# Performance work log

Measured on AMD Instinct MI355X. Metric: run time of the kernel, lower is better.

## Reference

```python
import jax, jax.numpy as jnp
from jax import lax
import numpy as np

B, S, E, HID = 16, 7, 64, 64
RES = (64, 64); D = RES[0] * RES[1]
XLOW, XHIGH = -0.5, 0.5
RLOW, RHIGH = float(np.sqrt(0.01)), float(np.sqrt(0.05))
PIXEL_MULT = 1.0; N_ITER = 3; TSOFT = 1.0 / float(np.sqrt(E))

def _build_grid():
    ranges = [np.linspace(XLOW, XHIGH, r) for r in RES]
    g = np.stack(np.meshgrid(*ranges, indexing='xy'), axis=-1)
    g = g.reshape(RES[0], RES[1], -1).reshape(1, -1, 2)
    return jnp.asarray(g, dtype=jnp.float32)

ABS_GRID = _build_grid()  # [1, D, 2]

def _ln(x, g, b):
    m = jnp.mean(x, -1, keepdims=True)
    v = jnp.mean(jnp.square(x - m), -1, keepdims=True)
    return (x - m) * lax.rsqrt(v + 1e-5) * g + b

def _forward(data, slot_noise, pos_rand, conv0_w, conv0_b, conv1_w, conv1_b, conv2_w, conv2_b,
             dataN_g, dataN_b, queryN_g, queryN_b, toK_w, toK_b, toV_w, toV_b, dense_w, dense_b,
             mlp1_w, mlp1_b, mlp2_w, mlp2_b, gru_wih, gru_whh, gru_bih, gru_bhh,
             alpha1_w, alpha1_b, alpha2_w, alpha2_b, final1_w, final1_b, final2_w, final2_b,
             slots_mu, slots_logsigma):
    dn = ('NCHW', 'OIHW', 'NCHW')
    def conv(x, w, b):
        return lax.conv_general_dilated(x, w, (1, 1), 'SAME', dimension_numbers=dn) + b[None, :, None, None]
    # CNN encoder: Conv-ReLU x3, 'same' padding, k=5
    x = jax.nn.relu(conv(data, conv0_w, conv0_b))
    x = jax.nn.relu(conv(x, conv1_w, conv1_b))
    x = jax.nn.relu(conv(x, conv2_w, conv2_b))
    enc = x.transpose(0, 2, 3, 1).reshape(B, D, HID)
    enc = _ln(enc, dataN_g, dataN_b)

    queries = slots_mu + jnp.exp(slots_logsigma) * slot_noise  # [B,S,E]
    # init_slots: faithful replication (source indexes the SLOT dim, and swaps rlow/rhigh)
    pos_scale = pos_rand.at[:, :2, :].add(-0.5)
    pos_scale = pos_scale.at[:, -1, :].set((RLOW - RHIGH) * pos_rand[:, -1, :] + RHIGH)

    encK = enc @ toK_w + toK_b  # [B,D,E]
    encV = enc @ toV_w + toV_b

    def init_mlp(y):
        y = _ln(y, queryN_g, queryN_b)
        return jax.nn.relu(y @ mlp1_w + mlp1_b) @ mlp2_w + mlp2_b

    def get_kv(ps):
        # per-slot relative grid: [B,S,D,2]
        rel = (ABS_GRID[:, None] - ps[:, :, None, :2]) / ps[:, :, -1][:, :, None, None]
        eg = PIXEL_MULT * (rel @ dense_w + dense_b)  # [B,S,D,E]
        return init_mlp(encK[:, None] + eg), init_mlp(encV[:, None] + eg)

    def att_wts(q, k):
        logits = jnp.einsum('bse,bsde->bsd', q, k) * TSOFT
        att = jax.nn.softmax(logits, axis=1)  # softmax over slots
        wts = att / jnp.sum(att, -1, keepdims=True) + 1e-8
        return att, wts

    def update_frames(wts):
        new_pos = jnp.einsum('bsd,de->bse', wts, ABS_GRID[0])  # [B,S,2]
        d2 = jnp.sum(jnp.square(ABS_GRID[:, None] - new_pos[:, :, None]), -1)  # [B,S,D]
        new_scale = jnp.sqrt(jnp.einsum('bsd,bsd->bs', wts, d2))
        return jnp.concatenate([new_pos, new_scale[..., None]], -1)

    def gru(xg, h):
        gi = xg @ gru_wih.T + gru_bih
        gh = h @ gru_whh.T + gru_bhh
        ir, iz, inn = jnp.split(gi, 3, -1)
        hr, hz, hn = jnp.split(gh, 3, -1)
        r = jax.nn.sigmoid(ir + hr)
        z = jax.nn.sigmoid(iz + hz)
        n = jnp.tanh(inn + r * hn)
        return (1.0 - z) * n + z * h

    for _ in range(N_ITER):
        keys, vals = get_kv(pos_scale)
        att, wts = att_wts(_ln(queries, queryN_g, queryN_b), keys)
        pos_scale = update_frames(wts)
        upd = jnp.einsum('bsd,bsde->bse', wts, vals)
        queries = gru(upd.reshape(-1, E), queries.reshape(-1, E)).reshape(B, S, E)

    keys, _ = get_kv(pos_scale)
    att, wts = att_wts(_ln(queries, queryN_g, queryN_b), keys)
    nps = update_frames(wts)
    alpha = jax.nn.sigmoid(jax.nn.relu(queries @ alpha1_w + alpha1_b) @ alpha2_w + alpha2_b)
    slot_feat = jax.nn.relu(queries @ final1_w + final1_b) @ final2_w + final2_b + nps
    return queries, att, slot_feat, alpha

def setup_inputs() -> dict:
    ks = jax.random.split(jax.random.key(0), 20)
    f32 = jnp.float32
    def rn(i, shape, s):
        return jax.random.normal(ks[i], shape, f32) * s
    inp = dict(
        data=jax.random.normal(ks[0], (B, 1, RES[0], RES[1]), f32),
        slot_noise=jax.random.normal(ks[1], (B, S, E), f32),
        pos_rand=jax.random.uniform(ks[2], (B, S, 3), dtype=f32),
        conv0_w=rn(3, (HID, 1, 5, 5), 0.2), conv0_b=jnp.zeros(HID, f32),
        conv1_w=rn(4, (HID, HID, 5, 5), 0.025), conv1_b=jnp.zeros(HID, f32),
        conv2_w=rn(5, (HID, HID, 5, 5), 0.025), conv2_b=jnp.zeros(HID, f32),
        dataN_g=jnp.ones(HID, f32), dataN_b=jnp.zeros(HID, f32),
        queryN_g=jnp.ones(E, f32), queryN_b=jnp.zeros(E, f32),
        toK_w=rn(6, (HID, E), 0.125), toK_b=jnp.zeros(E, f32),
        toV_w=rn(7, (HID, E), 0.125), toV_b=jnp.zeros(E, f32),
        dense_w=rn(8, (2, E), 0.7), dense_b=jnp.zeros(E, f32),
        mlp1_w=rn(9, (E, E), 0.125), mlp1_b=jnp.zeros(E, f32),
        mlp2_w=rn(10, (E, E), 0.125), mlp2_b=jnp.zeros(E, f32),
        gru_wih=rn(11, (3 * E, E), 0.125), gru_whh=rn(12, (3 * E, E), 0.125),
        gru_bih=jnp.zeros(3 * E, f32), gru_bhh=jnp.zeros(3 * E, f32),
        alpha1_w=rn(13, (E, 32), 0.125), alpha1_b=jnp.zeros(32, f32),
        alpha2_w=rn(14, (32, 1), 0.18), alpha2_b=jnp.zeros(1, f32),
        final1_w=rn(15, (E, HID), 0.125), final1_b=jnp.zeros(HID, f32),
        final2_w=rn(16, (HID, 3), 0.125), final2_b=jnp.zeros(3, f32),
        slots_mu=rn(17, (1, 1, E), 1.0),
        slots_logsigma=rn(18, (1, 1, E), 0.01),
    )
    return inp

def reference(data, slot_noise, pos_rand, conv0_w, conv0_b, conv1_w, conv1_b, conv2_w, conv2_b,
              dataN_g, dataN_b, queryN_g, queryN_b, toK_w, toK_b, toV_w, toV_b, dense_w, dense_b,
              mlp1_w, mlp1_b, mlp2_w, mlp2_b, gru_wih, gru_whh, gru_bih, gru_bhh,
              alpha1_w, alpha1_b, alpha2_w, alpha2_b, final1_w, final1_b, final2_w, final2_b,
              slots_mu, slots_logsigma):
    return _forward(data, slot_noise, pos_rand, conv0_w, conv0_b, conv1_w, conv1_b, conv2_w, conv2_b,
                    dataN_g, dataN_b, queryN_g, queryN_b, toK_w, toK_b, toV_w, toV_b, dense_w, dense_b,
                    mlp1_w, mlp1_b, mlp2_w, mlp2_b, gru_wih, gru_whh, gru_bih, gru_bhh,
                    alpha1_w, alpha1_b, alpha2_w, alpha2_b, final1_w, final1_b, final2_w, final2_b,
                    slots_mu, slots_logsigma)
```

## Files before the change

kernel.cpp:

```cpp
#include <hip/hip_runtime.h>
#include <cmath>


#define RLOW_F 0.1f
#define RHIGH_F 0.22360679774997896f
#define W0CONST 1.00004096f
#define SR2 704.3386243f

typedef __attribute__((ext_vector_type(8))) __bf16 bf16x8;
typedef __attribute__((ext_vector_type(4))) float f32x4;

__device__ __forceinline__ float wsum64(float v){
  #pragma unroll
  for (int off = 32; off > 0; off >>= 1) v += __shfl_xor(v, off, 64);
  return v;
}
__device__ __forceinline__ float rdlane(float v, int l){
  return __int_as_float(__builtin_amdgcn_readlane(__float_as_int(v), l));
}
__device__ __forceinline__ unsigned short bf16bits(float v){
  __bf16 h = (__bf16)v;
  return *reinterpret_cast<unsigned short*>(&h);
}

// ... 61 lines not shown
    int yy = y + r - 2, gx = cx - 2;
    float v = 0.f;
    if (yy >= 0 && yy < 64 && gx >= 0 && gx < 64) v = in[(b*64 + yy)*64 + gx];
    s_in[r*68 + cx] = v;
  }
  __syncthreads();
  int o = lane;
  float bvv = bias[o];
  float acc[16];
  #pragma unroll
  for (int k = 0; k < 16; k++) acc[k] = bvv;
  #pragma unroll
  for (int ky = 0; ky < 5; ky++){
    float rv[20];
    const float4* p = reinterpret_cast<const float4*>(&s_in[ky*68 + xg*16]);
    #pragma unroll
    for (int q = 0; q < 5; q++){ float4 f = p[q]; rv[q*4]=f.x; rv[q*4+1]=f.y; rv[q*4+2]=f.z; rv[q*4+3]=f.w; }
    #pragma unroll
    for (int kx = 0; kx < 5; kx++){
      float wv = s_w[o*25 + ky*5 + kx];
      #pragma unroll
      for (int k = 0; k < 16; k++) acc[k] = fmaf(rv[k+kx], wv, acc[k]);
    }
  }
  #pragma unroll
  for (int k = 0; k < 16; k++) s_out[o*65 + xg*16 + k] = fmaxf(acc[k], 0.f);
  __syncthreads();
  for (int i = t; i < 4096; i += 256){
    int px = i >> 6, ch = i & 63;
    out[((size_t)(b*64 + y)*64 + px)*64 + ch] = bf16bits(s_out[ch*65 + px]);
  }
}

__global__ void k_packconv(const float* __restrict__ w, unsigned short* __restrict__ out){
  int idx = blockIdx.x*256 + threadIdx.x;
  if (idx >= 102400) return;
  int j = idx & 7;
  int l = (idx >> 3) & 63;
  int frag = idx >> 9;
  int nt = frag & 3;
  int ks = (frag >> 2) % 10;
  int dy = frag / 40;
  int q = l >> 4, cr = l & 15;
  int k = ks*32 + q*8 + j;
  int kx = k >> 6, ch = k & 63;
  int n = nt*16 + cr;
  out[idx] = bf16bits(w[((n*64 + ch)*5 + dy)*5 + kx]);
}

__global__ __launch_bounds__(256) void k_convm(const unsigned short* __restrict__ in_bf,
                        const unsigned short* __restrict__ wpack,
                        const float* __restrict__ bias,
                        const float* __restrict__ lng, const float* __restrict__ lnb,
                        unsigned short* __restrict__ out_bf, float* __restrict__ out_f,
                        int mode){
  int bi = blockIdx.x;
  int b = bi >> 4; int yg = bi & 15;
  int t = threadIdx.x; int wv = t >> 6; int l = t & 63;
  int q = l >> 4, cr = l & 15;
  int p0 = wv*16;

  __shared__ char lds[8*68*144];

  for (int ri = 0; ri < 8; ri++){
    int yy = yg*4 + ri - 2;
    bool rok = (yy >= 0 && yy < 64);
    const uint4* src = reinterpret_cast<const uint4*>(in_bf + (size_t)(b*64 + yy)*64*64);
    for (int i = t; i < 544; i += 256){
      int px = i >> 3, c8 = i & 7;
      uint4 v = {0u,0u,0u,0u};
      int gx = px - 2;
      if (rok && gx >= 0 && gx < 64) v = src[gx*8 + c8];
      *reinterpret_cast<uint4*>(&lds[ri*9792 + px*144 + c8*16]) = v;
    }
  }
  __syncthreads();

  f32x4 acc[4][4];
  #pragma unroll
  for (int r = 0; r < 4; r++)
    #pragma unroll
    for (int nt = 0; nt < 4; nt++) acc[r][nt] = (f32x4){0.f,0.f,0.f,0.f};

  const bf16x8* wp = reinterpret_cast<const bf16x8*>(wpack);
  for (int dy = 0; dy < 5; dy++){
    for (int ks = 0; ks < 10; ks++){
      bf16x8 Bf[4];
      int fbase = (dy*10 + ks)*4;
      #pragma unroll
      for (int nt = 0; nt < 4; nt++) Bf[nt] = wp[(fbase + nt)*64 + l];
      int aoff = (p0 + cr + (ks >> 1))*144 + (ks & 1)*64 + q*16;
      #pragma unroll
      for (int r = 0; r < 4; r++){
        bf16x8 a = *reinterpret_cast<const bf16x8*>(&lds[(r + dy)*9792 + aoff]);
        #pragma unroll
        for (int nt = 0; nt < 4; nt++)
          acc[r][nt] = __builtin_amdgcn_mfma_f32_16x16x32_bf16(a, Bf[nt], acc[r][nt], 0, 0, 0);
      }
    }
  }

  float bvv[4];
  #pragma unroll
  for (int nt = 0; nt < 4; nt++) bvv[nt] = bias[nt*16 + cr];

  if (mode == 0){
    #pragma unroll
    for (int r = 0; r < 4; r++){
      int y = yg*4 + r;
      #pragma unroll
      for (int reg = 0; reg < 4; reg++){
        int p = p0 + q*4 + reg;
        size_t base = ((size_t)(b*64 + y)*64 + p)*64;
        #pragma unroll
        for (int nt = 0; nt < 4; nt++)
          out_bf[base + nt*16 + cr] = bf16bits(fmaxf(acc[r][nt][reg] + bvv[nt], 0.f));
      }
    }
  } else {
    float gv[4], bb[4];
    #pragma unroll
    for (int nt = 0; nt < 4; nt++){ gv[nt] = lng[nt*16 + cr]; bb[nt] = lnb[nt*16 + cr]; }
    #pragma unroll
    for (int r = 0; r < 4; r++){
      int y = yg*4 + r;
      #pragma unroll
      for (int reg = 0; reg < 4; reg++){
        int p = p0 + q*4 + reg;
        float v[4]; float s1 = 0.f, s2 = 0.f;
        #pragma unroll
        for (int nt = 0; nt < 4; nt++){
          v[nt] = fmaxf(acc[r][nt][reg] + bvv[nt], 0.f);
          s1 += v[nt]; s2 += v[nt]*v[nt];
        }
        #pragma unroll
        for (int m = 1; m < 16; m <<= 1){ s1 += __shfl_xor(s1, m, 64); s2 += __shfl_xor(s2, m, 64); }
        float mean = s1 * (1.f/64.f);
        float var  = s2 * (1.f/64.f) - mean*mean;
        float rstd = 1.0f/sqrtf(var + 1e-5f);
        size_t base = ((size_t)b*4096 + y*64 + p)*64;
        #pragma unroll
        for (int nt = 0; nt < 4; nt++)
          out_f[base + nt*16 + cr] = (v[nt] - mean)*rstd*gv[nt] + bb[nt];
      }
    }
  }
}

__global__ void k_packw1(const float* __restrict__ w1, unsigned short* __restrict__ out){
  int idx = blockIdx.x*256 + threadIdx.x;
  int jj = idx & 7;
  int lane = (idx >> 3) & 63;
  int frag = idx >> 9;
  int ks = frag >> 2, nt = frag & 3;
  int q = lane >> 4, cr = lane & 15;
  int k = ks*32 + q*8 + jj;
  int n = nt*16 + cr;
  out[idx] = bf16bits(w1[k*64 + n]);
}

__global__ __launch_bounds__(256) void k_projm(const float* __restrict__ enc,
                       const unsigned short* __restrict__ kpack, const float* __restrict__ bk,
                       const unsigned short* __restrict__ vpack, const float* __restrict__ bvp,
                       unsigned short* __restrict__ K, unsigned short* __restrict__ V){
  int bi = blockIdx.x; int b = bi >> 6; int tile = bi & 63;
  int t = threadIdx.x; int wv = t >> 6; int l = t & 63;
  int q = l >> 4, cr = l & 15;
  int d0 = tile*64 + wv*16;

  const bf16x8* kp = reinterpret_cast<const bf16x8*>(kpack);
  const bf16x8* vp = reinterpret_cast<const bf16x8*>(vpack);
  bf16x8 KB[8], VB[8];
  #pragma unroll
  for (int f = 0; f < 8; f++){ KB[f] = kp[f*64 + l]; VB[f] = vp[f*64 + l]; }

  const float* er = enc + (size_t)(b*4096 + d0 + cr)*64;
  bf16x8 a0, a1;
  #pragma unroll
  for (int h = 0; h < 2; h++){
    const float4* e4 = reinterpret_cast<const float4*>(er + (h ? (32 + q*8) : (q*8)));
    #pragma unroll
    for (int p = 0; p < 2; p++){
      float4 e = e4[p];
      if (h == 0){ a0[p*4+0]=(__bf16)e.x; a0[p*4+1]=(__bf16)e.y; a0[p*4+2]=(__bf16)e.z; a0[p*4+3]=(__bf16)e.w; }
      else       { a1[p*4+0]=(__bf16)e.x; a1[p*4+1]=(__bf16)e.y; a1[p*4+2]=(__bf16)e.z; a1[p*4+3]=(__bf16)e.w; }
    }
  }

  f32x4 zero = {0.f,0.f,0.f,0.f};
  f32x4 aK[4], aV[4];
  #pragma unroll
  for (int nt = 0; nt < 4; nt++){
    aK[nt] = __builtin_amdgcn_mfma_f32_16x16x32_bf16(a0, KB[nt],     zero,   0, 0, 0);
    aK[nt] = __builtin_amdgcn_mfma_f32_16x16x32_bf16(a1, KB[4 + nt], aK[nt], 0, 0, 0);
    aV[nt] = __builtin_amdgcn_mfma_f32_16x16x32_bf16(a0, VB[nt],     zero,   0, 0, 0);
    aV[nt] = __builtin_amdgcn_mfma_f32_16x16x32_bf16(a1, VB[4 + nt], aV[nt], 0, 0, 0);
  }
  #pragma unroll
  for (int nt = 0; nt < 4; nt++){
    float bkv = bk[nt*16 + cr], bvv = bvp[nt*16 + cr];
    #pragma unroll
    for (int reg = 0; reg < 4; reg++){
      size_t base = ((size_t)b*4096 + d0 + q*4 + reg)*64 + nt*16 + cr;
      K[base] = bf16bits(aK[nt][reg] + bkv);
      V[base] = bf16bits(aV[nt][reg] + bvv);
    }
  }
}

__global__ __launch_bounds__(256) void k_attnK(const unsigned short* __restrict__ encX,
     const unsigned short* __restrict__ w1pack, const float* __restrict__ mlp1b,
     const float* __restrict__ absc, const float* __restrict__ qg_,
     const float* __restrict__ qb_, const float* __restrict__ w2qc,
     float* __restrict__ att, float* __restrict__ accF){
  int bi = blockIdx.x;
  int b = bi >> 6, tile = bi & 63;
  int t = threadIdx.x; int wv = t >> 6; int l = t & 63;
  int q = l >> 4, cr = l & 15;
  int m0 = tile*64 + wv*16;
  int drow = m0 + cr;

  __shared__ float s_log[7*64];
  __shared__ float s_absc[7*192];
  __shared__ float s_wq[7*68];
  for (int i = t; i < 1344; i += 256) s_absc[i] = absc[b*7*192 + i];
  for (int i = t; i < 476;  i += 256) s_wq[i]   = w2qc[b*7*68 + i];

  const bf16x8* wp = reinterpret_cast<const bf16x8*>(w1pack);
  bf16x8 Bf[8];
  #pragma unroll
  for (int f = 0; f < 8; f++) Bf[f] = wp[f*64 + l];

  const unsigned short* er = encX + (size_t)(b*4096 + drow)*64;
  float gx = -0.5f + (float)(drow & 63) * (1.f/63.f);
  float gy = -0.5f + (float)((drow >> 6) & 63) * (1.f/63.f);
  float xb[16], gq[16], bq[16];
  {
    bf16x8 ea = *reinterpret_cast<const bf16x8*>(er + q*8);
    bf16x8 eb = *reinterpret_cast<const bf16x8*>(er + 32 + q*8);
    #pragma unroll
    for (int i = 0; i < 8; i++){ xb[i] = (float)ea[i]; xb[8+i] = (float)eb[i]; }
  }
  #pragma unroll
  for (int h = 0; h < 2; h++){
    int fb = h ? (32 + q*8) : (q*8);
    const float4* g4 = reinterpret_cast<const float4*>(qg_ + fb);
    const float4* b4 = reinterpret_cast<const float4*>(qb_ + fb);
    #pragma unroll
    for (int p = 0; p < 2; p++){
      float4 gg = g4[p], bb = b4[p];
      int o = h*8 + p*4;
      gq[o+0]=gg.x; gq[o+1]=gg.y; gq[o+2]=gg.z; gq[o+3]=gg.w;
      bq[o+0]=bb.x; bq[o+1]=bb.y; bq[o+2]=bb.z; bq[o+3]=bb.w;
    }
  }
  float b1v[4];
  #pragma unroll
  for (int nt = 0; nt < 4; nt++) b1v[nt] = mlp1b[nt*16 + cr];
  __syncthreads();

  for (int s = 0; s < 7; s++){
    const float* Ac = s_absc + s*192;
    float x[16];
    #pragma unroll
    for (int h = 0; h < 2; h++){
      int fb = h ? (32 + q*8) : (q*8);
      const float4* A4 = reinterpret_cast<const float4*>(Ac + fb);
      const float4* B4 = reinterpret_cast<const float4*>(Ac + 64 + fb);
      const float4* C4 = reinterpret_cast<const float4*>(Ac + 128 + fb);
      #pragma unroll
      for (int p = 0; p < 2; p++){
        float4 Av = A4[p], Bv = B4[p], Cv = C4[p];
        int o = h*8 + p*4;
        x[o+0] = xb[o+0] + gx*Av.x + gy*Bv.x + Cv.x;
        x[o+1] = xb[o+1] + gx*Av.y + gy*Bv.y + Cv.y;
        x[o+2] = xb[o+2] + gx*Av.z + gy*Bv.z + Cv.z;
        x[o+3] = xb[o+3] + gx*Av.w + gy*Bv.w + Cv.w;
      }
    }
    float sum = 0.f;
    #pragma unroll
    for (int k = 0; k < 16; k++) sum += x[k];
    sum += __shfl_xor(sum, 16, 64); sum += __shfl_xor(sum, 32, 64);
    float m = sum * (1.f/64.f);
    float v = 0.f;
    #pragma unroll
    for (int k = 0; k < 16; k++){ float dd = x[k] - m; v += dd*dd; }
    v += __shfl_xor(v, 16, 64); v += __shfl_xor(v, 32, 64);
    float rstd = 1.0f/sqrtf(v * (1.f/64.f) + 1e-5f);

    bf16x8 a0, a1;
    #pragma unroll
    for (int k = 0; k < 8; k++)  a0[k] = (__bf16)((x[k]   - m)*rstd*gq[k]   + bq[k]);
    #pragma unroll
    for (int k = 0; k < 8; k++)  a1[k] = (__bf16)((x[8+k] - m)*rstd*gq[8+k] + bq[8+k]);

    f32x4 zero = {0.f, 0.f, 0.f, 0.f};
    f32x4 acc[4];
    #pragma unroll
    for (int nt = 0; nt < 4; nt++){
      acc[nt] = __builtin_amdgcn_mfma_f32_16x16x32_bf16(a0, Bf[nt],     zero,    0, 0, 0);
      acc[nt] = __builtin_amdgcn_mfma_f32_16x16x32_bf16(a1, Bf[4 + nt], acc[nt], 0, 0, 0);
    }

    float c2 = s_wq[s*68 + 64];
    float p[4] = {0.f, 0.f, 0.f, 0.f};
    #pragma unroll
    for (int nt = 0; nt < 4; nt++){
      float wqv = s_wq[s*68 + nt*16 + cr];
      #pragma unroll
      for (int reg = 0; reg < 4; reg++){
        float y = fmaxf(acc[nt][reg] + b1v[nt], 0.f);
        p[reg] = fmaf(y, wqv, p[reg]);
      }
    }
    #pragma unroll
    for (int reg = 0; reg < 4; reg++){
      #pragma unroll
      for (int off = 1; off < 16; off <<= 1) p[reg] += __shfl_xor(p[reg], off, 64);
    }
    if (cr == 0){
      #pragma unroll
      for (int reg = 0; reg < 4; reg++)
        s_log[s*64 + wv*16 + q*4 + reg] = (p[reg] + c2) * 0.125f;
    }
  }
  __syncthreads();

  if (t < 64){
    float lv[7];
    #pragma unroll
    for (int s = 0; s < 7; s++) lv[s] = s_log[s*64 + t];
    float mx = lv[0];
    #pragma unroll
    for (int s = 1; s < 7; s++) mx = fmaxf(mx, lv[s]);
    float sm = 0.f;
    #pragma unroll
    for (int s = 0; s < 7; s++){ lv[s] = expf(lv[s] - mx); sm += lv[s]; }
    float inv = 1.0f / sm;
    #pragma unroll
    for (int s = 0; s < 7; s++){
      float a = lv[s] * inv;
      s_log[s*64 + t] = a;
      att[(size_t)(b*7+s)*4096 + tile*64 + t] = a;
    }
  }
  __syncthreads();

  if (t < 224){
    int s = t >> 5, r = t & 31;
    float a1 = s_log[s*64 + r];
    float a2 = s_log[s*64 + r + 32];
    float gx1 = -0.5f + (float)r * (1.f/63.f);
    float gx2 = -0.5f + (float)(r + 32) * (1.f/63.f);
    float gyc = -0.5f + (float)tile * (1.f/63.f);
    float gy2c = gyc*gyc;
    float w0 = a1 + a2;
    float w1 = a1*gx1 + a2*gx2;
    float w2 = w0*gyc;
    float w3 = a1*(gx1*gx1 + gy2c) + a2*(gx2*gx2 + gy2c);
    #pragma unroll
    for (int m = 1; m < 32; m <<= 1){
      w0 += __shfl_xor(w0, m, 64);
      w1 += __shfl_xor(w1, m, 64);
      w2 += __shfl_xor(w2, m, 64);
      w3 += __shfl_xor(w3, m, 64);
    }
    if (r == 0){
      atomicAdd(&accF[(b*7+s)*4 + 0], w0);
      atomicAdd(&accF[(b*7+s)*4 + 1], w1);
      atomicAdd(&accF[(b*7+s)*4 + 2], w2);
      atomicAdd(&accF[(b*7+s)*4 + 3], w3);
    }
  }
}

__global__ __launch_bounds__(256) void k_attnV(const unsigned short* __restrict__ encX,
     const unsigned short* __restrict__ w1pack, const float* __restrict__ mlp1b,
     const float* __restrict__ absc, const float* __restrict__ qg_,
     const float* __restrict__ qb_, const float* __restrict__ att,
     const float* __restrict__ accF, float* __restrict__ upd){
  int bi = blockIdx.x;
  int b = bi >> 6, tile = bi & 63;
  int t = threadIdx.x; int wv = t >> 6; int l = t & 63;
  int q = l >> 4, cr = l & 15;
  int m0 = tile*64 + wv*16;
  int drow = m0 + cr;

  __shared__ float s_absc[7*192];
  __shared__ float s_att[7*64];
  __shared__ float s_upd[7*64];
  __shared__ float s_inv[7];
  for (int i = t; i < 1344; i += 256) s_absc[i] = absc[b*7*192 + i];
  for (int i = t; i < 448;  i += 256){
    s_att[i] = att[(size_t)(b*7 + (i >> 6))*4096 + tile*64 + (i & 63)];
    s_upd[i] = 0.f;
  }
  if (t < 7) s_inv[t] = 1.0f / accF[(b*7 + t)*4];

  const bf16x8* wp = reinterpret_cast<const bf16x8*>(w1pack);
  bf16x8 Bf[8];
  #pragma unroll
  for (int f = 0; f < 8; f++) Bf[f] = wp[f*64 + l];

  const unsigned short* er = encX + (size_t)(b*4096 + drow)*64;
  float gx = -0.5f + (float)(drow & 63) * (1.f/63.f);
  float gy = -0.5f + (float)((drow >> 6) & 63) * (1.f/63.f);
  float xb[16], gq[16], bq[16];
  {
    bf16x8 ea = *reinterpret_cast<const bf16x8*>(er + q*8);
    bf16x8 eb = *reinterpret_cast<const bf16x8*>(er + 32 + q*8);
    #pragma unroll
    for (int i = 0; i < 8; i++){ xb[i] = (float)ea[i]; xb[8+i] = (float)eb[i]; }
  }
  #pragma unroll
  for (int h = 0; h < 2; h++){
    int fb = h ? (32 + q*8) : (q*8);
    const float4* g4 = reinterpret_cast<const float4*>(qg_ + fb);
    const float4* b4 = reinterpret_cast<const float4*>(qb_ + fb);
    #pragma unroll
    for (int p = 0; p < 2; p++){
      float4 gg = g4[p], bb = b4[p];
      int o = h*8 + p*4;
      gq[o+0]=gg.x; gq[o+1]=gg.y; gq[o+2]=gg.z; gq[o+3]=gg.w;
      bq[o+0]=bb.x; bq[o+1]=bb.y; bq[o+2]=bb.z; bq[o+3]=bb.w;
    }
  }
  float b1v[4];
  #pragma unroll
  for (int nt = 0; nt < 4; nt++) b1v[nt] = mlp1b[nt*16 + cr];
  __syncthreads();

  for (int s = 0; s < 7; s++){
    const float* Ac = s_absc + s*192;
    float x[16];
    #pragma unroll
    for (int h = 0; h < 2; h++){
      int fb = h ? (32 + q*8) : (q*8);
      const float4* A4 = reinterpret_cast<const float4*>(Ac + fb);
      const float4* B4 = reinterpret_cast<const float4*>(Ac + 64 + fb);
      const float4* C4 = reinterpret_cast<const float4*>(Ac + 128 + fb);
      #pragma unroll
      for (int p = 0; p < 2; p++){
        float4 Av = A4[p], Bv = B4[p], Cv = C4[p];
        int o = h*8 + p*4;
        x[o+0] = xb[o+0] + gx*Av.x + gy*Bv.x + Cv.x;
        x[o+1] = xb[o+1] + gx*Av.y + gy*Bv.y + Cv.y;
        x[o+2] = xb[o+2] + gx*Av.z + gy*Bv.z + Cv.z;
        x[o+3] = xb[o+3] + gx*Av.w + gy*Bv.w + Cv.w;
      }
    }
    float sum = 0.f;
    #pragma unroll
    for (int k = 0; k < 16; k++) sum += x[k];
    sum += __shfl_xor(sum, 16, 64); sum += __shfl_xor(sum, 32, 64);
    float m = sum * (1.f/64.f);
    float v = 0.f;
    #pragma unroll
    for (int k = 0; k < 16; k++){ float dd = x[k] - m; v += dd*dd; }
    v += __shfl_xor(v, 16, 64); v += __shfl_xor(v, 32, 64);
    float rstd = 1.0f/sqrtf(v * (1.f/64.f) + 1e-5f);

    bf16x8 a0, a1;
    #pragma unroll
    for (int k = 0; k < 8; k++)  a0[k] = (__bf16)((x[k]   - m)*rstd*gq[k]   + bq[k]);
    #pragma unroll
    for (int k = 0; k < 8; k++)  a1[k] = (__bf16)((x[8+k] - m)*rstd*gq[8+k] + bq[8+k]);

    f32x4 zero = {0.f, 0.f, 0.f, 0.f};
    f32x4 acc[4];
    #pragma unroll
    for (int nt = 0; nt < 4; nt++){
      acc[nt] = __builtin_amdgcn_mfma_f32_16x16x32_bf16(a0, Bf[nt],     zero,    0, 0, 0);
      acc[nt] = __builtin_amdgcn_mfma_f32_16x16x32_bf16(a1, Bf[4 + nt], acc[nt], 0, 0, 0);
    }

    float rsa = s_inv[s];
    float wr[4];
    #pragma unroll
    for (int reg = 0; reg < 4; reg++)
      wr[reg] = fmaf(s_att[s*64 + wv*16 + q*4 + reg], rsa, 1e-8f);
    float pc[4];
    #pragma unroll
    for (int nt = 0; nt < 4; nt++){
      pc[nt] = 0.f;
      #pragma unroll
      for (int reg = 0; reg < 4; reg++)
        pc[nt] = fmaf(wr[reg], fmaxf(acc[nt][reg] + b1v[nt], 0.f), pc[nt]);
    }
    #pragma unroll
    for (int nt = 0; nt < 4; nt++){
      pc[nt] += __shfl_xor(pc[nt], 16, 64);
      pc[nt] += __shfl_xor(pc[nt], 32, 64);
    }
    if (q == 0){
      #pragma unroll
      for (int nt = 0; nt < 4; nt++)
        atomicAdd(&s_upd[s*64 + nt*16 + cr], pc[nt]);
    }
  }
  __syncthreads();
  for (int i = t; i < 448; i += 256)
    atomicAdd(&upd[b*448 + i], s_upd[i]);
}

__global__ void k_gru(float* __restrict__ upd, float* __restrict__ queries,
                      const float* __restrict__ wih, const float* __restrict__ whh,
                      const float* __restrict__ bih, const float* __restrict__ bhh,
                      const float* __restrict__ mlp2w, const float* __restrict__ mlp2b,
                      float* __restrict__ accF, float* __restrict__ ps,
                      const float* __restrict__ qg_, const float* __restrict__ qb_,
                      const float* __restrict__ dw, const float* __restrict__ db,
                      float* __restrict__ absc, float* __restrict__ w2qc){
  int row = blockIdx.x; int t = threadIdx.x;
  __shared__ float us[64], hs[64], xs[64], gis[192], ghs[192];
  __shared__ float s_ps3[3];
  if (t < 64){ us[t] = upd[row*64 + t]; hs[t] = queries[row*64 + t]; }
  if (t == 64){
    float sa = accF[row*4+0];
    float ax = accF[row*4+1], ay = accF[row*4+2], ar2 = accF[row*4+3];
    float isa = 1.0f/sa;
    float Wx = ax*isa, Wy = ay*isa;
    float Wg = ar2*isa + 1e-8f*SR2;
    float s2 = Wg - (Wx*Wx + Wy*Wy)*(2.f - W0CONST);
    s_ps3[0] = Wx; s_ps3[1] = Wy; s_ps3[2] = sqrtf(fmaxf(s2, 0.f));
  }
  __syncthreads();
  if (t < 64){
    float a = W0CONST * mlp2b[t];
    for (int i = 0; i < 64; i++) a = fmaf(us[i], mlp2w[i*64 + t], a);
    xs[t] = a;
  }
  __syncthreads();
  float gi = bih[t], gh = bhh[t];
  for (int e = 0; e < 64; e++){
    gi = fmaf(wih[t*64 + e], xs[e], gi);
    gh = fmaf(whh[t*64 + e], hs[e], gh);
  }
  gis[t] = gi; ghs[t] = gh;
  __syncthreads();
  if (t < 64){
    float r = 1.0f/(1.0f + expf(-(gis[t]      + ghs[t])));
    float z = 1.0f/(1.0f + expf(-(gis[64+t]   + ghs[64+t])));
    float n = tanhf(gis[128+t] + r*ghs[128+t]);
    float newq = (1.0f - z)*n + z*hs[t];
    queries[row*64 + t] = newq;
    upd[row*64 + t] = 0.f;
    if (t < 4) accF[row*4 + t] = 0.f;
    if (t < 3) ps[row*3 + t] = s_ps3[t];
    pp_core(row, t, newq, s_ps3[0], s_ps3[1], s_ps3[2],
            qg_, qb_, dw, db, mlp2w, mlp2b, absc, w2qc);
  }
}

__global__ void k_final(const float* __restrict__ queries, const float* __restrict__ accF,
                        const float* __restrict__ a1w, const float* __restrict__ a1b,
// ... 44 lines not shown
  const float* conv0_b     = (const float*)d_in[4];
  const float* conv1_w     = (const float*)d_in[5];
  const float* conv1_b     = (const float*)d_in[6];
  const float* conv2_w     = (const float*)d_in[7];
  const float* conv2_b     = (const float*)d_in[8];
  const float* dataN_g     = (const float*)d_in[9];
  const float* dataN_b     = (const float*)d_in[10];
  const float* queryN_g    = (const float*)d_in[11];
  const float* queryN_b    = (const float*)d_in[12];
  const float* toK_w       = (const float*)d_in[13];
  const float* toK_b       = (const float*)d_in[14];
  const float* toV_w       = (const float*)d_in[15];
  const float* toV_b       = (const float*)d_in[16];
  const float* dense_w     = (const float*)d_in[17];
  const float* dense_b     = (const float*)d_in[18];
  const float* mlp1_w      = (const float*)d_in[19];
  const float* mlp1_b      = (const float*)d_in[20];
  const float* mlp2_w      = (const float*)d_in[21];
  const float* mlp2_b      = (const float*)d_in[22];
  const float* gru_wih     = (const float*)d_in[23];
  const float* gru_whh     = (const float*)d_in[24];
  const float* gru_bih     = (const float*)d_in[25];
  const float* gru_bhh     = (const float*)d_in[26];
  const float* alpha1_w    = (const float*)d_in[27];
  const float* alpha1_b    = (const float*)d_in[28];
  const float* alpha2_w    = (const float*)d_in[29];
  const float* alpha2_b    = (const float*)d_in[30];
  const float* final1_w    = (const float*)d_in[31];
  const float* final1_b    = (const float*)d_in[32];
  const float* final2_w    = (const float*)d_in[33];
  const float* final2_b    = (const float*)d_in[34];
  const float* slots_mu    = (const float*)d_in[35];
  const float* slots_lsig  = (const float*)d_in[36];

  float* ws   = (float*)d_ws;
  float* bufA = ws;
  float* bufB = bufA + 4194304;
  float* bufC = bufB + 4194304;
  float* attw = bufC + 4194304;
  float* queries = attw + 458752;
  float* ps   = queries + 7168;
  float* absc = ps + 512;
  float* accF = absc + 21504;
  float* upd  = accF + 512;
  float* w2qc = upd + 7168;
  unsigned short* w1pack = (unsigned short*)(w2qc + 7616);
  unsigned short* kpack  = w1pack + 4096;
  unsigned short* vpack  = kpack + 4096;
  unsigned short* wp1    = vpack + 4096;
  unsigned short* wp2    = wp1 + 102400;

  unsigned short* c0_bf = (unsigned short*)bufA;
  unsigned short* c1_bf = (unsigned short*)bufC;
  float* enc = bufB;
  unsigned short* encK = (unsigned short*)bufA;
  unsigned short* encV = (unsigned short*)bufC;

  float* outq   = (float*)d_out;
  float* outatt = outq + 7168;

  k_prep<<<112, 64, 0, stream>>>(slot_noise, pos_rand, slots_mu, slots_lsig,
                                 queryN_g, queryN_b, dense_w, dense_b, mlp2_w, mlp2_b,
                                 queries, ps, absc, w2qc, accF, upd);
  k_packw1<<<16, 256, 0, stream>>>(mlp1_w, w1pack);
  k_packw1<<<16, 256, 0, stream>>>(toK_w, kpack);
  k_packw1<<<16, 256, 0, stream>>>(toV_w, vpack);
  k_packconv<<<400, 256, 0, stream>>>(conv1_w, wp1);
  k_packconv<<<400, 256, 0, stream>>>(conv2_w, wp2);
  k_conv0<<<1024, 256, 0, stream>>>(data, conv0_w, conv0_b, c0_bf);
  k_convm<<<256, 256, 0, stream>>>(c0_bf, wp1, conv1_b, nullptr, nullptr, c1_bf, nullptr, 0);
  k_convm<<<256, 256, 0, stream>>>(c1_bf, wp2, conv2_b, dataN_g, dataN_b, nullptr, enc, 1);
  k_projm<<<1024, 256, 0, stream>>>(enc, kpack, toK_b, vpack, toV_b, encK, encV);

  for (int p = 0; p < 4; p++){
    float* attp = (p == 3) ? outatt : attw;
    k_attnK<<<1024, 256, 0, stream>>>(encK, w1pack, mlp1_b, absc, queryN_g, queryN_b,
                                      w2qc, attp, accF);
    if (p < 3){
      k_attnV<<<1024, 256, 0, stream>>>(encV, w1pack, mlp1_b, absc, queryN_g, queryN_b,
                                        attp, accF, upd);
      k_gru<<<112, 192, 0, stream>>>(upd, queries, gru_wih, gru_whh, gru_bih, gru_bhh,
                                     mlp2_w, mlp2_b, accF, ps, queryN_g, queryN_b,
                                     dense_w, dense_b, absc, w2qc);
    }
  }
  k_final<<<112, 64, 0, stream>>>(queries, accF,
                                  alpha1_w, alpha1_b, alpha2_w, alpha2_b,
                                  final1_w, final1_b, final2_w, final2_b, outq);
}
```

Baseline: 535.2 us.

## Split attention kernels per slot, add separate softmax kernel, halve conv tiles

The fused per-batch attention kernels, which looped over the 7 slots serially, become per-(batch,slot) kernels launched with 7x more blocks. Softmax and the attention-moment reductions move into a new small k_softfr kernel that reads the logits back from global memory. The conv kernel is split along x into twice as many blocks with smaller LDS tiles. The layer-normed encoder output is now stored as bf16 instead of fp32, so the projection kernel loads bf16 directly. The intent is better GPU occupancy and latency hiding. The costs are 7x redundant reads of encoder rows, an extra kernel launch per iteration, and more global atomics.

```diff
diff --git a/kernel.cpp b/kernel.cpp
--- a/kernel.cpp
+++ b/kernel.cpp
@@ -137,33 +137,33 @@
                         const unsigned short* __restrict__ wpack,
                         const float* __restrict__ bias,
                         const float* __restrict__ lng, const float* __restrict__ lnb,
-                        unsigned short* __restrict__ out_bf, float* __restrict__ out_f,
-                        int mode){
+                        unsigned short* __restrict__ out_bf, int mode){
   int bi = blockIdx.x;
-  int b = bi >> 4; int yg = bi & 15;
+  int b = bi >> 5; int yg = (bi >> 1) & 15; int xh = bi & 1;
   int t = threadIdx.x; int wv = t >> 6; int l = t & 63;
   int q = l >> 4, cr = l & 15;
-  int p0 = wv*16;
-
-  __shared__ char lds[8*68*144];
+  int yr = wv >> 1, ph = wv & 1;
+  int p0 = ph*16;
+
+  __shared__ char lds[8*36*144];
 
   for (int ri = 0; ri < 8; ri++){
     int yy = yg*4 + ri - 2;
     bool rok = (yy >= 0 && yy < 64);
     const uint4* src = reinterpret_cast<const uint4*>(in_bf + (size_t)(b*64 + yy)*64*64);
-    for (int i = t; i < 544; i += 256){
+    for (int i = t; i < 288; i += 256){
       int px = i >> 3, c8 = i & 7;
       uint4 v = {0u,0u,0u,0u};
-      int gx = px - 2;
+      int gx = xh*32 + px - 2;
       if (rok && gx >= 0 && gx < 64) v = src[gx*8 + c8];
-      *reinterpret_cast<uint4*>(&lds[ri*9792 + px*144 + c8*16]) = v;
-    }
-  }
-  __syncthreads();
-
-  f32x4 acc[4][4];
-  #pragma unroll
-  for (int r = 0; r < 4; r++)
+      *reinterpret_cast<uint4*>(&lds[ri*5184 + px*144 + c8*16]) = v;
+    }
+  }
+  __syncthreads();
+
+  f32x4 acc[2][4];
+  #pragma unroll
+  for (int r = 0; r < 2; r++)
     #pragma unroll
     for (int nt = 0; nt < 4; nt++) acc[r][nt] = (f32x4){0.f,0.f,0.f,0.f};
 
@@ -176,8 +176,9 @@
       for (int nt = 0; nt < 4; nt++) Bf[nt] = wp[(fbase + nt)*64 + l];
       int aoff = (p0 + cr + (ks >> 1))*144 + (ks & 1)*64 + q*16;
       #pragma unroll
-      for (int r = 0; r < 4; r++){
-        bf16x8 a = *reinterpret_cast<const bf16x8*>(&lds[(r + dy)*9792 + aoff]);
+      for (int r = 0; r < 2; r++){
+        int ri = yr*2 + r + dy;
+        bf16x8 a = *reinterpret_cast<const bf16x8*>(&lds[ri*5184 + aoff]);
         #pragma unroll
         for (int nt = 0; nt < 4; nt++)
           acc[r][nt] = __builtin_amdgcn_mfma_f32_16x16x32_bf16(a, Bf[nt], acc[r][nt], 0, 0, 0);
@@ -191,11 +192,11 @@
 
   if (mode == 0){
     #pragma unroll
-    for (int r = 0; r < 4; r++){
-      int y = yg*4 + r;
+    for (int r = 0; r < 2; r++){
+      int y = yg*4 + yr*2 + r;
       #pragma unroll
       for (int reg = 0; reg < 4; reg++){
-        int p = p0 + q*4 + reg;
+        int p = xh*32 + p0 + q*4 + reg;
         size_t base = ((size_t)(b*64 + y)*64 + p)*64;
         #pragma unroll
         for (int nt = 0; nt < 4; nt++)
@@ -207,11 +208,11 @@
     #pragma unroll
     for (int nt = 0; nt < 4; nt++){ gv[nt] = lng[nt*16 + cr]; bb[nt] = lnb[nt*16 + cr]; }
     #pragma unroll
-    for (int r = 0; r < 4; r++){
-      int y = yg*4 + r;
+    for (int r = 0; r < 2; r++){
+      int y = yg*4 + yr*2 + r;
       #pragma unroll
       for (int reg = 0; reg < 4; reg++){
-        int p = p0 + q*4 + reg;
+        int p = xh*32 + p0 + q*4 + reg;
         float v[4]; float s1 = 0.f, s2 = 0.f;
         #pragma unroll
         for (int nt = 0; nt < 4; nt++){
@@ -226,7 +227,7 @@
         size_t base = ((size_t)b*4096 + y*64 + p)*64;
         #pragma unroll
         for (int nt = 0; nt < 4; nt++)
-          out_f[base + nt*16 + cr] = (v[nt] - mean)*rstd*gv[nt] + bb[nt];
+          out_bf[base + nt*16 + cr] = bf16bits((v[nt] - mean)*rstd*gv[nt] + bb[nt]);
       }
     }
   }
@@ -244,7 +245,7 @@
   out[idx] = bf16bits(w1[k*64 + n]);
 }
 
-__global__ __launch_bounds__(256) void k_projm(const float* __restrict__ enc,
+__global__ __launch_bounds__(256) void k_projm(const unsigned short* __restrict__ enc,
                        const unsigned short* __restrict__ kpack, const float* __restrict__ bk,
                        const unsigned short* __restrict__ vpack, const float* __restrict__ bvp,
                        unsigned short* __restrict__ K, unsigned short* __restrict__ V){
@@ -259,18 +260,9 @@
   #pragma unroll
   for (int f = 0; f < 8; f++){ KB[f] = kp[f*64 + l]; VB[f] = vp[f*64 + l]; }
 
-  const float* er = enc + (size_t)(b*4096 + d0 + cr)*64;
-  bf16x8 a0, a1;
-  #pragma unroll
-  for (int h = 0; h < 2; h++){
-    const float4* e4 = reinterpret_cast<const float4*>(er + (h ? (32 + q*8) : (q*8)));
-    #pragma unroll
-    for (int p = 0; p < 2; p++){
-      float4 e = e4[p];
-      if (h == 0){ a0[p*4+0]=(__bf16)e.x; a0[p*4+1]=(__bf16)e.y; a0[p*4+2]=(__bf16)e.z; a0[p*4+3]=(__bf16)e.w; }
-      else       { a1[p*4+0]=(__bf16)e.x; a1[p*4+1]=(__bf16)e.y; a1[p*4+2]=(__bf16)e.z; a1[p*4+3]=(__bf16)e.w; }
-    }
-  }
+  const unsigned short* er = enc + (size_t)(b*4096 + d0 + cr)*64;
+  bf16x8 a0 = *reinterpret_cast<const bf16x8*>(er + q*8);
+  bf16x8 a1 = *reinterpret_cast<const bf16x8*>(er + 32 + q*8);
 
   f32x4 zero = {0.f,0.f,0.f,0.f};
   f32x4 aK[4], aV[4];
@@ -293,165 +285,133 @@
   }
 }
 
-__global__ __launch_bounds__(256) void k_attnK(const unsigned short* __restrict__ encX,
+__global__ __launch_bounds__(256) void k_attnK7(const unsigned short* __restrict__ encX,
      const unsigned short* __restrict__ w1pack, const float* __restrict__ mlp1b,
      const float* __restrict__ absc, const float* __restrict__ qg_,
      const float* __restrict__ qb_, const float* __restrict__ w2qc,
-     float* __restrict__ att, float* __restrict__ accF){
+     float* __restrict__ logits){
   int bi = blockIdx.x;
-  int b = bi >> 6, tile = bi & 63;
+  int tile = bi & 63; int bs = bi >> 6;
+  int b = bs / 7;
   int t = threadIdx.x; int wv = t >> 6; int l = t & 63;
   int q = l >> 4, cr = l & 15;
   int m0 = tile*64 + wv*16;
   int drow = m0 + cr;
 
-  __shared__ float s_log[7*64];
-  __shared__ float s_absc[7*192];
-  __shared__ float s_wq[7*68];
-  for (int i = t; i < 1344; i += 256) s_absc[i] = absc[b*7*192 + i];
-  for (int i = t; i < 476;  i += 256) s_wq[i]   = w2qc[b*7*68 + i];
-
   const bf16x8* wp = reinterpret_cast<const bf16x8*>(w1pack);
   bf16x8 Bf[8];
   #pragma unroll
   for (int f = 0; f < 8; f++) Bf[f] = wp[f*64 + l];
 
+  const float* Ac = absc + bs*192;
   const unsigned short* er = encX + (size_t)(b*4096 + drow)*64;
   float gx = -0.5f + (float)(drow & 63) * (1.f/63.f);
   float gy = -0.5f + (float)((drow >> 6) & 63) * (1.f/63.f);
-  float xb[16], gq[16], bq[16];
+  float x[16];
   {
     bf16x8 ea = *reinterpret_cast<const bf16x8*>(er + q*8);
     bf16x8 eb = *reinterpret_cast<const bf16x8*>(er + 32 + q*8);
     #pragma unroll
-    for (int i = 0; i < 8; i++){ xb[i] = (float)ea[i]; xb[8+i] = (float)eb[i]; }
-  }
+    for (int i = 0; i < 8; i++){ x[i] = (float)ea[i]; x[8+i] = (float)eb[i]; }
+  }
+  float gq[16], bq[16];
   #pragma unroll
   for (int h = 0; h < 2; h++){
     int fb = h ? (32 + q*8) : (q*8);
+    const float4* A4 = reinterpret_cast<const float4*>(Ac + fb);
+    const float4* B4 = reinterpret_cast<const float4*>(Ac + 64 + fb);
+    const float4* C4 = reinterpret_cast<const float4*>(Ac + 128 + fb);
     const float4* g4 = reinterpret_cast<const float4*>(qg_ + fb);
     const float4* b4 = reinterpret_cast<const float4*>(qb_ + fb);
     #pragma unroll
     for (int p = 0; p < 2; p++){
-      float4 gg = g4[p], bb = b4[p];
+      float4 Av = A4[p], Bv = B4[p], Cv = C4[p], gg = g4[p], bb = b4[p];
       int o = h*8 + p*4;
+      x[o+0] += gx*Av.x + gy*Bv.x + Cv.x;
+      x[o+1] += gx*Av.y + gy*Bv.y + Cv.y;
+      x[o+2] += gx*Av.z + gy*Bv.z + Cv.z;
+      x[o+3] += gx*Av.w + gy*Bv.w + Cv.w;
       gq[o+0]=gg.x; gq[o+1]=gg.y; gq[o+2]=gg.z; gq[o+3]=gg.w;
       bq[o+0]=bb.x; bq[o+1]=bb.y; bq[o+2]=bb.z; bq[o+3]=bb.w;
     }
   }
-  float b1v[4];
-  #pragma unroll
-  for (int nt = 0; nt < 4; nt++) b1v[nt] = mlp1b[nt*16 + cr];
-  __syncthreads();
-
+  float s1 = 0.f, s2 = 0.f;
+  #pragma unroll
+  for (int k = 0; k < 16; k++){ s1 += x[k]; s2 = fmaf(x[k], x[k], s2); }
+  s1 += __shfl_xor(s1, 16, 64); s2 += __shfl_xor(s2, 16, 64);
+  s1 += __shfl_xor(s1, 32, 64); s2 += __shfl_xor(s2, 32, 64);
+  float m = s1 * (1.f/64.f);
+  float rstd = 1.0f/sqrtf(s2*(1.f/64.f) - m*m + 1e-5f);
+
+  bf16x8 a0, a1;
+  #pragma unroll
+  for (int k = 0; k < 8; k++){
+    a0[k] = (__bf16)((x[k]   - m)*rstd*gq[k]   + bq[k]);
+    a1[k] = (__bf16)((x[8+k] - m)*rstd*gq[8+k] + bq[8+k]);
+  }
+
+  f32x4 zero = {0.f, 0.f, 0.f, 0.f};
+  f32x4 acc[4];
+  #pragma unroll
+  for (int nt = 0; nt < 4; nt++){
+    acc[nt] = __builtin_amdgcn_mfma_f32_16x16x32_bf16(a0, Bf[nt],     zero,    0, 0, 0);
+    acc[nt] = __builtin_amdgcn_mfma_f32_16x16x32_bf16(a1, Bf[4 + nt], acc[nt], 0, 0, 0);
+  }
+
+  const float* wq = w2qc + bs*68;
+  float c2 = wq[64];
+  float p[4] = {0.f, 0.f, 0.f, 0.f};
+  #pragma unroll
+  for (int nt = 0; nt < 4; nt++){
+    float bb  = mlp1b[nt*16 + cr];
+    float wqv = wq[nt*16 + cr];
+    #pragma unroll
+    for (int reg = 0; reg < 4; reg++){
+      float y = fmaxf(acc[nt][reg] + bb, 0.f);
+      p[reg] = fmaf(y, wqv, p[reg]);
+    }
+  }
+  #pragma unroll
+  for (int reg = 0; reg < 4; reg++){
+    #pragma unroll
+    for (int off = 1; off < 16; off <<= 1) p[reg] += __shfl_xor(p[reg], off, 64);
+  }
+  if (cr == 0){
+    #pragma unroll
+    for (int reg = 0; reg < 4; reg++)
+      logits[(size_t)bs*4096 + m0 + q*4 + reg] = (p[reg] + c2) * 0.125f;
+  }
+}
+
+__global__ void k_softfr(const float* __restrict__ logits, float* __restrict__ attout,
+                         float* __restrict__ accF){
+  int bi = blockIdx.x;
+  int b = bi >> 4;
+  int t = threadIdx.x;
+  int d = (bi & 15)*256 + t;
+  int lane = t & 63;
+  float lv[7];
+  #pragma unroll
+  for (int s = 0; s < 7; s++) lv[s] = logits[(size_t)(b*7+s)*4096 + d];
+  float mx = lv[0];
+  #pragma unroll
+  for (int s = 1; s < 7; s++) mx = fmaxf(mx, lv[s]);
+  float sm = 0.f;
+  #pragma unroll
+  for (int s = 0; s < 7; s++){ lv[s] = expf(lv[s] - mx); sm += lv[s]; }
+  float inv = 1.0f / sm;
+  float gx = -0.5f + (float)(d & 63) * (1.f/63.f);
+  float gy = -0.5f + (float)(d >> 6) * (1.f/63.f);
+  float r2 = gx*gx + gy*gy;
+  #pragma unroll
   for (int s = 0; s < 7; s++){
-    const float* Ac = s_absc + s*192;
-    float x[16];
-    #pragma unroll
-    for (int h = 0; h < 2; h++){
-      int fb = h ? (32 + q*8) : (q*8);
-      const float4* A4 = reinterpret_cast<const float4*>(Ac + fb);
-      const float4* B4 = reinterpret_cast<const float4*>(Ac + 64 + fb);
-      const float4* C4 = reinterpret_cast<const float4*>(Ac + 128 + fb);
-      #pragma unroll
-      for (int p = 0; p < 2; p++){
-        float4 Av = A4[p], Bv = B4[p], Cv = C4[p];
-        int o = h*8 + p*4;
-        x[o+0] = xb[o+0] + gx*Av.x + gy*Bv.x + Cv.x;
-        x[o+1] = xb[o+1] + gx*Av.y + gy*Bv.y + Cv.y;
-        x[o+2] = xb[o+2] + gx*Av.z + gy*Bv.z + Cv.z;
-        x[o+3] = xb[o+3] + gx*Av.w + gy*Bv.w + Cv.w;
-      }
-    }
-    float sum = 0.f;
-    #pragma unroll
-    for (int k = 0; k < 16; k++) sum += x[k];
-    sum += __shfl_xor(sum, 16, 64); sum += __shfl_xor(sum, 32, 64);
-    float m = sum * (1.f/64.f);
-    float v = 0.f;
-    #pragma unroll
-    for (int k = 0; k < 16; k++){ float dd = x[k] - m; v += dd*dd; }
-    v += __shfl_xor(v, 16, 64); v += __shfl_xor(v, 32, 64);
-    float rstd = 1.0f/sqrtf(v * (1.f/64.f) + 1e-5f);
-
-    bf16x8 a0, a1;
-    #pragma unroll
-    for (int k = 0; k < 8; k++)  a0[k] = (__bf16)((x[k]   - m)*rstd*gq[k]   + bq[k]);
-    #pragma unroll
-    for (int k = 0; k < 8; k++)  a1[k] = (__bf16)((x[8+k] - m)*rstd*gq[8+k] + bq[8+k]);
-
-    f32x4 zero = {0.f, 0.f, 0.f, 0.f};
-    f32x4 acc[4];
-    #pragma unroll
-    for (int nt = 0; nt < 4; nt++){
-      acc[nt] = __builtin_amdgcn_mfma_f32_16x16x32_bf16(a0, Bf[nt],     zero,    0, 0, 0);
-      acc[nt] = __builtin_amdgcn_mfma_f32_16x16x32_bf16(a1, Bf[4 + nt], acc[nt], 0, 0, 0);
-    }
-
-    float c2 = s_wq[s*68 + 64];
-    float p[4] = {0.f, 0.f, 0.f, 0.f};
-    #pragma unroll
-    for (int nt = 0; nt < 4; nt++){
-      float wqv = s_wq[s*68 + nt*16 + cr];
-      #pragma unroll
-      for (int reg = 0; reg < 4; reg++){
-        float y = fmaxf(acc[nt][reg] + b1v[nt], 0.f);
-        p[reg] = fmaf(y, wqv, p[reg]);
-      }
-    }
-    #pragma unroll
-    for (int reg = 0; reg < 4; reg++){
-      #pragma unroll
-      for (int off = 1; off < 16; off <<= 1) p[reg] += __shfl_xor(p[reg], off, 64);
-    }
-    if (cr == 0){
-      #pragma unroll
-      for (int reg = 0; reg < 4; reg++)
-        s_log[s*64 + wv*16 + q*4 + reg] = (p[reg] + c2) * 0.125f;
-    }
-  }
-  __syncthreads();
-
-  if (t < 64){
-    float lv[7];
-    #pragma unroll
-    for (int s = 0; s < 7; s++) lv[s] = s_log[s*64 + t];
-    float mx = lv[0];
-    #pragma unroll
-    for (int s = 1; s < 7; s++) mx = fmaxf(mx, lv[s]);
-    float sm = 0.f;
-    #pragma unroll
-    for (int s = 0; s < 7; s++){ lv[s] = expf(lv[s] - mx); sm += lv[s]; }
-    float inv = 1.0f / sm;
-    #pragma unroll
-    for (int s = 0; s < 7; s++){
-      float a = lv[s] * inv;
-      s_log[s*64 + t] = a;
-      att[(size_t)(b*7+s)*4096 + tile*64 + t] = a;
-    }
-  }
-  __syncthreads();
-
-  if (t < 224){
-    int s = t >> 5, r = t & 31;
-    float a1 = s_log[s*64 + r];
-    float a2 = s_log[s*64 + r + 32];
-    float gx1 = -0.5f + (float)r * (1.f/63.f);
-    float gx2 = -0.5f + (float)(r + 32) * (1.f/63.f);
-    float gyc = -0.5f + (float)tile * (1.f/63.f);
-    float gy2c = gyc*gyc;
-    float w0 = a1 + a2;
-    float w1 = a1*gx1 + a2*gx2;
-    float w2 = w0*gyc;
-    float w3 = a1*(gx1*gx1 + gy2c) + a2*(gx2*gx2 + gy2c);
-    #pragma unroll
-    for (int m = 1; m < 32; m <<= 1){
-      w0 += __shfl_xor(w0, m, 64);
-      w1 += __shfl_xor(w1, m, 64);
-      w2 += __shfl_xor(w2, m, 64);
-      w3 += __shfl_xor(w3, m, 64);
-    }
-    if (r == 0){
+    float a = lv[s] * inv;
+    attout[(size_t)(b*7+s)*4096 + d] = a;
+    float w0 = wsum64(a);
+    float w1 = wsum64(a*gx);
+    float w2 = wsum64(a*gy);
+    float w3 = wsum64(a*r2);
+    if (lane == 0){
       atomicAdd(&accF[(b*7+s)*4 + 0], w0);
       atomicAdd(&accF[(b*7+s)*4 + 1], w1);
       atomicAdd(&accF[(b*7+s)*4 + 2], w2);
@@ -460,133 +420,106 @@
   }
 }
 
-__global__ __launch_bounds__(256) void k_attnV(const unsigned short* __restrict__ encX,
+__global__ __launch_bounds__(256) void k_attnV7(const unsigned short* __restrict__ encX,
      const unsigned short* __restrict__ w1pack, const float* __restrict__ mlp1b,
      const float* __restrict__ absc, const float* __restrict__ qg_,
      const float* __restrict__ qb_, const float* __restrict__ att,
      const float* __restrict__ accF, float* __restrict__ upd){
   int bi = blockIdx.x;
-  int b = bi >> 6, tile = bi & 63;
+  int tile = bi & 63; int bs = bi >> 6;
+  int b = bs / 7;
   int t = threadIdx.x; int wv = t >> 6; int l = t & 63;
   int q = l >> 4, cr = l & 15;
   int m0 = tile*64 + wv*16;
   int drow = m0 + cr;
 
-  __shared__ float s_absc[7*192];
-  __shared__ float s_att[7*64];
-  __shared__ float s_upd[7*64];
-  __shared__ float s_inv[7];
-  for (int i = t; i < 1344; i += 256) s_absc[i] = absc[b*7*192 + i];
-  for (int i = t; i < 448;  i += 256){
-    s_att[i] = att[(size_t)(b*7 + (i >> 6))*4096 + tile*64 + (i & 63)];
-    s_upd[i] = 0.f;
-  }
-  if (t < 7) s_inv[t] = 1.0f / accF[(b*7 + t)*4];
+  __shared__ float red[4][64];
 
   const bf16x8* wp = reinterpret_cast<const bf16x8*>(w1pack);
   bf16x8 Bf[8];
   #pragma unroll
   for (int f = 0; f < 8; f++) Bf[f] = wp[f*64 + l];
 
+  const float* Ac = absc + bs*192;
   const unsigned short* er = encX + (size_t)(b*4096 + drow)*64;
   float gx = -0.5f + (float)(drow & 63) * (1.f/63.f);
   float gy = -0.5f + (float)((drow >> 6) & 63) * (1.f/63.f);
-  float xb[16], gq[16], bq[16];
+  float x[16];
   {
     bf16x8 ea = *reinterpret_cast<const bf16x8*>(er + q*8);
     bf16x8 eb = *reinterpret_cast<const bf16x8*>(er + 32 + q*8);
     #pragma unroll
-    for (int i = 0; i < 8; i++){ xb[i] = (float)ea[i]; xb[8+i] = (float)eb[i]; }
-  }
+    for (int i = 0; i < 8; i++){ x[i] = (float)ea[i]; x[8+i] = (float)eb[i]; }
+  }
+  float gq[16], bq[16];
   #pragma unroll
   for (int h = 0; h < 2; h++){
     int fb = h ? (32 + q*8) : (q*8);
+    const float4* A4 = reinterpret_cast<const float4*>(Ac + fb);
+    const float4* B4 = reinterpret_cast<const float4*>(Ac + 64 + fb);
+    const float4* C4 = reinterpret_cast<const float4*>(Ac + 128 + fb);
     const float4* g4 = reinterpret_cast<const float4*>(qg_ + fb);
     const float4* b4 = reinterpret_cast<const float4*>(qb_ + fb);
     #pragma unroll
     for (int p = 0; p < 2; p++){
-      float4 gg = g4[p], bb = b4[p];
+      float4 Av = A4[p], Bv = B4[p], Cv = C4[p], gg = g4[p], bb = b4[p];
       int o = h*8 + p*4;
+      x[o+0] += gx*Av.x + gy*Bv.x + Cv.x;
+      x[o+1] += gx*Av.y + gy*Bv.y + Cv.y;
+      x[o+2] += gx*Av.z + gy*Bv.z + Cv.z;
+      x[o+3] += gx*Av.w + gy*Bv.w + Cv.w;
       gq[o+0]=gg.x; gq[o+1]=gg.y; gq[o+2]=gg.z; gq[o+3]=gg.w;
       bq[o+0]=bb.x; bq[o+1]=bb.y; bq[o+2]=bb.z; bq[o+3]=bb.w;
     }
   }
-  float b1v[4];
-  #pragma unroll
-  for (int nt = 0; nt < 4; nt++) b1v[nt] = mlp1b[nt*16 + cr];
-  __syncthreads();
-
-  for (int s = 0; s < 7; s++){
-    const float* Ac = s_absc + s*192;
-    float x[16];
-    #pragma unroll
-    for (int h = 0; h < 2; h++){
-      int fb = h ? (32 + q*8) : (q*8);
-      const float4* A4 = reinterpret_cast<const float4*>(Ac + fb);
-      const float4* B4 = reinterpret_cast<const float4*>(Ac + 64 + fb);
-      const float4* C4 = reinterpret_cast<const float4*>(Ac + 128 + fb);
-      #pragma unroll
-      for (int p = 0; p < 2; p++){
-        float4 Av = A4[p], Bv = B4[p], Cv = C4[p];
-        int o = h*8 + p*4;
-        x[o+0] = xb[o+0] + gx*Av.x + gy*Bv.x + Cv.x;
-        x[o+1] = xb[o+1] + gx*Av.y + gy*Bv.y + Cv.y;
-        x[o+2] = xb[o+2] + gx*Av.z + gy*Bv.z + Cv.z;
-        x[o+3] = xb[o+3] + gx*Av.w + gy*Bv.w + Cv.w;
-      }
-    }
-    float sum = 0.f;
-    #pragma unroll
-    for (int k = 0; k < 16; k++) sum += x[k];
-    sum += __shfl_xor(sum, 16, 64); sum += __shfl_xor(sum, 32, 64);
-    float m = sum * (1.f/64.f);
-    float v = 0.f;
-    #pragma unroll
-    for (int k = 0; k < 16; k++){ float dd = x[k] - m; v += dd*dd; }
-    v += __shfl_xor(v, 16, 64); v += __shfl_xor(v, 32, 64);
-    float rstd = 1.0f/sqrtf(v * (1.f/64.f) + 1e-5f);
-
-    bf16x8 a0, a1;
-    #pragma unroll
-    for (int k = 0; k < 8; k++)  a0[k] = (__bf16)((x[k]   - m)*rstd*gq[k]   + bq[k]);
-    #pragma unroll
-    for (int k = 0; k < 8; k++)  a1[k] = (__bf16)((x[8+k] - m)*rstd*gq[8+k] + bq[8+k]);
-
-    f32x4 zero = {0.f, 0.f, 0.f, 0.f};
-    f32x4 acc[4];
-    #pragma unroll
-    for (int nt = 0; nt < 4; nt++){
-      acc[nt] = __builtin_amdgcn_mfma_f32_16x16x32_bf16(a0, Bf[nt],     zero,    0, 0, 0);
-      acc[nt] = __builtin_amdgcn_mfma_f32_16x16x32_bf16(a1, Bf[4 + nt], acc[nt], 0, 0, 0);
-    }
-
-    float rsa = s_inv[s];
-    float wr[4];
+  float s1 = 0.f, s2 = 0.f;
+  #pragma unroll
+  for (int k = 0; k < 16; k++){ s1 += x[k]; s2 = fmaf(x[k], x[k], s2); }
+  s1 += __shfl_xor(s1, 16, 64); s2 += __shfl_xor(s2, 16, 64);
+  s1 += __shfl_xor(s1, 32, 64); s2 += __shfl_xor(s2, 32, 64);
+  float m = s1 * (1.f/64.f);
+  float rstd = 1.0f/sqrtf(s2*(1.f/64.f) - m*m + 1e-5f);
+
+  bf16x8 a0, a1;
+  #pragma unroll
+  for (int k = 0; k < 8; k++){
+    a0[k] = (__bf16)((x[k]   - m)*rstd*gq[k]   + bq[k]);
+    a1[k] = (__bf16)((x[8+k] - m)*rstd*gq[8+k] + bq[8+k]);
+  }
+
+  f32x4 zero = {0.f, 0.f, 0.f, 0.f};
+  f32x4 acc[4];
+  #pragma unroll
+  for (int nt = 0; nt < 4; nt++){
+    acc[nt] = __builtin_amdgcn_mfma_f32_16x16x32_bf16(a0, Bf[nt],     zero,    0, 0, 0);
+    acc[nt] = __builtin_amdgcn_mfma_f32_16x16x32_bf16(a1, Bf[4 + nt], acc[nt], 0, 0, 0);
+  }
+
+  float isa = 1.0f / accF[bs*4];
+  float wr[4];
+  #pragma unroll
+  for (int reg = 0; reg < 4; reg++)
+    wr[reg] = fmaf(att[(size_t)bs*4096 + m0 + q*4 + reg], isa, 1e-8f);
+  float pc[4];
+  #pragma unroll
+  for (int nt = 0; nt < 4; nt++){
+    pc[nt] = 0.f;
+    float bb = mlp1b[nt*16 + cr];
     #pragma unroll
     for (int reg = 0; reg < 4; reg++)
-      wr[reg] = fmaf(s_att[s*64 + wv*16 + q*4 + reg], rsa, 1e-8f);
-    float pc[4];
-    #pragma unroll
-    for (int nt = 0; nt < 4; nt++){
-      pc[nt] = 0.f;
-      #pragma unroll
-      for (int reg = 0; reg < 4; reg++)
-        pc[nt] = fmaf(wr[reg], fmaxf(acc[nt][reg] + b1v[nt], 0.f), pc[nt]);
-    }
-    #pragma unroll
-    for (int nt = 0; nt < 4; nt++){
-      pc[nt] += __shfl_xor(pc[nt], 16, 64);
-      pc[nt] += __shfl_xor(pc[nt], 32, 64);
-    }
-    if (q == 0){
-      #pragma unroll
-      for (int nt = 0; nt < 4; nt++)
-        atomicAdd(&s_upd[s*64 + nt*16 + cr], pc[nt]);
-    }
-  }
-  __syncthreads();
-  for (int i = t; i < 448; i += 256)
-    atomicAdd(&upd[b*448 + i], s_upd[i]);
+      pc[nt] = fmaf(wr[reg], fmaxf(acc[nt][reg] + bb, 0.f), pc[nt]);
+  }
+  #pragma unroll
+  for (int nt = 0; nt < 4; nt++){
+    pc[nt] += __shfl_xor(pc[nt], 16, 64);
+    pc[nt] += __shfl_xor(pc[nt], 32, 64);
+  }
+  if (q == 0){
+    #pragma unroll
+    for (int nt = 0; nt < 4; nt++) red[wv][nt*16 + cr] = pc[nt];
+  }
+  __syncthreads();
+  if (t < 64) atomicAdd(&upd[bs*64 + t], red[0][t] + red[1][t] + red[2][t] + red[3][t]);
 }
 
 __global__ void k_gru(float* __restrict__ upd, float* __restrict__ queries,
@@ -737,9 +670,9 @@
 
   unsigned short* c0_bf = (unsigned short*)bufA;
   unsigned short* c1_bf = (unsigned short*)bufC;
-  float* enc = bufB;
-  unsigned short* encK = (unsigned short*)bufA;
-  unsigned short* encV = (unsigned short*)bufC;
+  unsigned short* enc   = (unsigned short*)bufB;
+  unsigned short* encK  = (unsigned short*)bufA;
+  unsigned short* encV  = (unsigned short*)bufC;
 
   float* outq   = (float*)d_out;
   float* outatt = outq + 7168;
@@ -753,17 +686,18 @@
   k_packconv<<<400, 256, 0, stream>>>(conv1_w, wp1);
   k_packconv<<<400, 256, 0, stream>>>(conv2_w, wp2);
   k_conv0<<<1024, 256, 0, stream>>>(data, conv0_w, conv0_b, c0_bf);
-  k_convm<<<256, 256, 0, stream>>>(c0_bf, wp1, conv1_b, nullptr, nullptr, c1_bf, nullptr, 0);
-  k_convm<<<256, 256, 0, stream>>>(c1_bf, wp2, conv2_b, dataN_g, dataN_b, nullptr, enc, 1);
+  k_convm<<<512, 256, 0, stream>>>(c0_bf, wp1, conv1_b, nullptr, nullptr, c1_bf, 0);
+  k_convm<<<512, 256, 0, stream>>>(c1_bf, wp2, conv2_b, dataN_g, dataN_b, enc, 1);
   k_projm<<<1024, 256, 0, stream>>>(enc, kpack, toK_b, vpack, toV_b, encK, encV);
 
   for (int p = 0; p < 4; p++){
     float* attp = (p == 3) ? outatt : attw;
-    k_attnK<<<1024, 256, 0, stream>>>(encK, w1pack, mlp1_b, absc, queryN_g, queryN_b,
-                                      w2qc, attp, accF);
+    k_attnK7<<<7168, 256, 0, stream>>>(encK, w1pack, mlp1_b, absc, queryN_g, queryN_b,
+                                       w2qc, attw);
+    k_softfr<<<256, 256, 0, stream>>>(attw, attp, accF);
     if (p < 3){
-      k_attnV<<<1024, 256, 0, stream>>>(encV, w1pack, mlp1_b, absc, queryN_g, queryN_b,
-                                        attp, accF, upd);
+      k_attnV7<<<7168, 256, 0, stream>>>(encV, w1pack, mlp1_b, absc, queryN_g, queryN_b,
+                                         attp, accF, upd);
       k_gru<<<112, 192, 0, stream>>>(upd, queries, gru_wih, gru_whh, gru_bih, gru_bhh,
                                      mlp2_w, mlp2_b, accF, ps, queryN_g, queryN_b,
                                      dense_w, dense_b, absc, w2qc);
```

Result: slower. 584.3 us (+9.2%).
